# Optimization experiments

Measured on AMD Instinct MI355X. Metric: run time of the kernel, lower is better.

## Reference

```python
import jax, jax.numpy as jnp
import numpy as np

NUM_HEADS = 16


def setup_inputs() -> dict:
    key = jax.random.key(0)
    ks = jax.random.split(key, 5)
    B, S, D = 4, 2048, 1024
    scale = 1.0 / np.sqrt(D)
    return {
        "x": jax.random.normal(ks[0], (B, S, D), dtype=jnp.float32),
        "q_proj": jax.random.normal(ks[1], (D, D), dtype=jnp.float32) * scale,
        "k_proj": jax.random.normal(ks[2], (D, D), dtype=jnp.float32) * scale,
        "v_proj": jax.random.normal(ks[3], (D, D), dtype=jnp.float32) * scale,
        "o_proj": jax.random.normal(ks[4], (D, D), dtype=jnp.float32) * scale,
    }


def reference(x, q_proj, k_proj, v_proj, o_proj):
    B, S, D = x.shape
    H = NUM_HEADS
    hd = D // H
    # projections: weight is [d_out, d_in]
    q = jnp.einsum('bsd,kd->bsk', x, q_proj)
    k = jnp.einsum('bsd,kd->bsk', x, k_proj)
    v = jnp.einsum('bsd,kd->bsk', x, v_proj)
    # split heads: [B, H, S, hd]
    q = q.reshape(B, S, H, hd).transpose(0, 2, 1, 3)
    k = k.reshape(B, S, H, hd).transpose(0, 2, 1, 3)
    v = v.reshape(B, S, H, hd).transpose(0, 2, 1, 3)
    scores = jnp.einsum('bhqd,bhkd->bhqk', q, k) / jnp.sqrt(jnp.asarray(hd, dtype=x.dtype))
    causal = jnp.tril(jnp.ones((S, S), dtype=bool))  # True = keep
    scores = jnp.where(causal, scores, -jnp.inf)
    attn = jax.nn.softmax(scores, axis=-1)
    out = jnp.einsum('bhqk,bhkd->bhqd', attn, v)
    out = out.transpose(0, 2, 1, 3).reshape(B, S, D)
    return jnp.einsum('bsv,mv->bsm', out, o_proj)
```

## Files before the change

### kernel.cpp

```cpp
#include <hip/hip_runtime.h>
#include <hip/hip_bf16.h>
#include <stdint.h>


typedef __bf16 bf16x8 __attribute__((ext_vector_type(8)));
typedef __bf16 bf16x4 __attribute__((ext_vector_type(4)));
typedef float  f32x4  __attribute__((ext_vector_type(4)));

static __device__ __forceinline__ f32x4 mfma16(bf16x8 a, bf16x8 b, f32x4 c) {
  return __builtin_amdgcn_mfma_f32_16x16x32_bf16(a, b, c, 0, 0, 0);
}

static __device__ __forceinline__ void load16_lds(const void* g, void* l) {
  __builtin_amdgcn_global_load_lds(
      (const __attribute__((address_space(1))) unsigned int*)g,
      (__attribute__((address_space(3))) unsigned int*)l, 16, 0, 0);
}

__global__ __launch_bounds__(256) void cvt_all(
    const float* __restrict__ x,
    const float* __restrict__ w0, const float* __restrict__ w1,
    const float* __restrict__ w2, const float* __restrict__ w3,
    __bf16* __restrict__ xb, __bf16* __restrict__ wqk,
    __bf16* __restrict__ wvb, __bf16* __restrict__ wob) {
  const int blk = blockIdx.x;
  const int t = threadIdx.x;
  if (blk < 4096) {
    int i = blk * 256 + t;
    const float4* in4 = (const float4*)x;
    float4 a = in4[2 * i], b = in4[2 * i + 1];
    __bf16 v[8];
    v[0] = (__bf16)a.x; v[1] = (__bf16)a.y; v[2] = (__bf16)a.z; v[3] = (__bf16)a.w;
    v[4] = (__bf16)b.x; v[5] = (__bf16)b.y; v[6] = (__bf16)b.z; v[7] = (__bf16)b.w;
    *(bf16x8*)(xb + 8 * i) = *(bf16x8*)v;
  } else {
    int b2 = blk - 4096;
    int m = b2 >> 9;
    const float* src = (m == 0) ? w0 : (m == 1) ? w1 : (m == 2) ? w2 : w3;
    __bf16* dst = (m == 0) ? wqk : (m == 1) ? (wqk + (size_t)(1024 * 1024))
                : (m == 2) ? wvb : wob;
    const float scl = (m == 0) ? 0.18033688011112042f : 1.0f;
    int i = (b2 & 511) * 256 + t;
    const float4* in4 = (const float4*)src;
    float4 a = in4[2 * i], b = in4[2 * i + 1];
    __bf16 v[8];
    v[0] = (__bf16)(a.x * scl); v[1] = (__bf16)(a.y * scl);
    v[2] = (__bf16)(a.z * scl); v[3] = (__bf16)(a.w * scl);
    v[4] = (__bf16)(b.x * scl); v[5] = (__bf16)(b.y * scl);
    v[6] = (__bf16)(b.z * scl); v[7] = (__bf16)(b.w * scl);
    *(bf16x8*)(dst + 8 * i) = *(bf16x8*)v;
  }
}

static __device__ __forceinline__ void stage_unit(
    const __bf16* __restrict__ X, long grow0, int K, long k0,
    __bf16* lds, int t) {
  const int lane = t & 63, w = t >> 6;
  const int rl = w * 8 + (lane >> 3);
  const int chunk = (lane & 7) ^ ((lane >> 3) & 7);
  load16_lds(X + (grow0 + rl) * (long)K + k0 + chunk * 8,
             lds + (w * 8) * 64);
}

template <typename OutT>
static __device__ __forceinline__ void gemm_core(
    const __bf16* __restrict__ A, const __bf16* __restrict__ Bw,
    OutT* __restrict__ C, int N, int K, long m0, long n0, int t) {
  __shared__ __align__(16) __bf16 As[3][256 * 64];
  __shared__ __align__(16) __bf16 Bs[3][128 * 64];
  const int lane = t & 63, w = t >> 6;
  const int wm = w >> 1, wn = w & 1;
  const int l15 = lane & 15, quad = lane >> 4;

  int aoff[4][2], boff[4][2];
#pragma unroll
  for (int mf = 0; mf < 4; mf++)
#pragma unroll
    for (int ks = 0; ks < 2; ks++)
      aoff[mf][ks] = (wm * 64 + mf * 16 + l15) * 64 + (((ks * 4 + quad) ^ (l15 & 7)) << 3);
#pragma unroll
  for (int nf = 0; nf < 4; nf++)
#pragma unroll
    for (int ks = 0; ks < 2; ks++)
      boff[nf][ks] = (wn * 64 + nf * 16 + l15) * 64 + (((ks * 4 + quad) ^ (l15 & 7)) << 3);

  const int NT = K >> 6;
  __bf16 *Ac = As[0], *An = As[1], *Asg = As[2];
  __bf16 *Bc = Bs[0], *Bn = Bs[1], *Bsg = Bs[2];

#pragma unroll
  for (int u = 0; u < 4; u++) stage_unit(A, m0 + u * 64, K, 0, Ac + u * 64 * 64, t);
#pragma unroll
  for (int u = 0; u < 2; u++) stage_unit(Bw, n0 + u * 64, K, 0, Bc + u * 64 * 64, t);
#pragma unroll
  for (int u = 0; u < 4; u++) stage_unit(A, m0 + u * 64, K, 64, An + u * 64 * 64, t);
#pragma unroll
  for (int u = 0; u < 2; u++) stage_unit(Bw, n0 + u * 64, K, 64, Bn + u * 64 * 64, t);
  asm volatile("s_waitcnt vmcnt(6)" ::: "memory");
  __builtin_amdgcn_s_barrier();

  f32x4 acc[4][4] = {};
  for (int T = 0; T < NT; T++) {
    const bool pf2 = (T + 2 < NT);
    const long kn2 = (long)(T + 2) * 64;

    bf16x8 bfr[4][2];
#pragma unroll
    for (int nf = 0; nf < 4; nf++)
#pragma unroll
      for (int ks = 0; ks < 2; ks++)
        bfr[nf][ks] = *(const bf16x8*)(Bc + boff[nf][ks]);
    {
      bf16x8 a00 = *(const bf16x8*)(Ac + aoff[0][0]);
      bf16x8 a01 = *(const bf16x8*)(Ac + aoff[0][1]);
      bf16x8 a10 = *(const bf16x8*)(Ac + aoff[1][0]);
      bf16x8 a11 = *(const bf16x8*)(Ac + aoff[1][1]);
      if (pf2) {
#pragma unroll
        for (int u = 0; u < 4; u++)
          stage_unit(A, m0 + u * 64, K, kn2, Asg + u * 64 * 64, t);
      }
      __builtin_amdgcn_s_barrier();
      asm volatile("s_waitcnt lgkmcnt(0)" ::: "memory");
      __builtin_amdgcn_sched_barrier(0);
      __builtin_amdgcn_s_setprio(1);
#pragma unroll
      for (int nf = 0; nf < 4; nf++) {
        acc[0][nf] = mfma16(a00, bfr[nf][0], acc[0][nf]);
        acc[0][nf] = mfma16(a01, bfr[nf][1], acc[0][nf]);
        acc[1][nf] = mfma16(a10, bfr[nf][0], acc[1][nf]);
        acc[1][nf] = mfma16(a11, bfr[nf][1], acc[1][nf]);
      }
      __builtin_amdgcn_s_setprio(0);
      __builtin_amdgcn_s_barrier();
    }
    {
      bf16x8 a00 = *(const bf16x8*)(Ac + aoff[2][0]);
      bf16x8 a01 = *(const bf16x8*)(Ac + aoff[2][1]);
      bf16x8 a10 = *(const bf16x8*)(Ac + aoff[3][0]);
      bf16x8 a11 = *(const bf16x8*)(Ac + aoff[3][1]);
      if (pf2) {
#pragma unroll
        for (int u = 0; u < 2; u++)
          stage_unit(Bw, n0 + u * 64, K, kn2, Bsg + u * 64 * 64, t);
        asm volatile("s_waitcnt vmcnt(6)" ::: "memory");
      } else {
        asm volatile("s_waitcnt vmcnt(0)" ::: "memory");
      }
      __builtin_amdgcn_s_barrier();
      asm volatile("s_waitcnt lgkmcnt(0)" ::: "memory");
      __builtin_amdgcn_sched_barrier(0);
      __builtin_amdgcn_s_setprio(1);
#pragma unroll
      for (int nf = 0; nf < 4; nf++) {
        acc[2][nf] = mfma16(a00, bfr[nf][0], acc[2][nf]);
        acc[2][nf] = mfma16(a01, bfr[nf][1], acc[2][nf]);
        acc[3][nf] = mfma16(a10, bfr[nf][0], acc[3][nf]);
        acc[3][nf] = mfma16(a11, bfr[nf][1], acc[3][nf]);
      }
      __builtin_amdgcn_s_setprio(0);
      __builtin_amdgcn_s_barrier();
    }
    __bf16* ta = Ac; Ac = An; An = Asg; Asg = ta;
    __bf16* tb = Bc; Bc = Bn; Bn = Bsg; Bsg = tb;
  }

#pragma unroll
  for (int mf = 0; mf < 4; mf++)
#pragma unroll
    for (int nf = 0; nf < 4; nf++)
#pragma unroll
      for (int r = 0; r < 4; r++) {
        long row = m0 + wm * 64 + mf * 16 + quad * 4 + r;
        long col = n0 + wn * 64 + nf * 16 + l15;
        float v = acc[mf][nf][r];
        if constexpr (sizeof(OutT) == 2) C[row * (long)N + col] = (OutT)(__bf16)v;
        else                             C[row * (long)N + col] = v;
      }
}

__global__ __launch_bounds__(512, 2) void gemm_dual(
    const __bf16* __restrict__ xb, const __bf16* __restrict__ wqk,
    const __bf16* __restrict__ wvb,
    __bf16* __restrict__ QK, __bf16* __restrict__ VTg) {
  const int bid = blockIdx.x;
  const int swz = (bid & 7) * 96 + (bid >> 3);
  if (swz < 512) {
    gemm_core<__bf16>(xb, wqk, QK, 2048, 1024,
                      (long)(swz / 16) * 256, (long)(swz % 16) * 128, threadIdx.x);
  } else {
    const int s = swz - 512;
    gemm_core<__bf16>(wvb, xb, VTg, 8192, 1024,
                      (long)(s / 64) * 256, (long)(s % 64) * 128, threadIdx.x);
  }
}

__global__ __launch_bounds__(512, 2) void gemm_bt8(
    const __bf16* __restrict__ A, const __bf16* __restrict__ Bw,
    float* __restrict__ C, int M, int N, int K, int NX) {
  const int bid = blockIdx.x;
  const int cpx = gridDim.x >> 3;
  const int swz = (bid & 7) * cpx + (bid >> 3);
  gemm_core<float>(A, Bw, C, N, K, (long)(swz / NX) * 256, (long)(swz % NX) * 128,
                   threadIdx.x);
}

__global__ __launch_bounds__(512, 2) void attn6(
    const __bf16* __restrict__ QK, const __bf16* __restrict__ VT,
    __bf16* __restrict__ O) {
  constexpr int SD = 2048;
  constexpr int LDP = 72;
  __shared__ __align__(16) __bf16 Ks[3][64 * 64];
  __shared__ __align__(16) __bf16 Vs[3][64 * 64];
  __shared__ __align__(16) __bf16 Pw[8 * 32 * LDP];
  const int t = threadIdx.x;
  const int lane = t & 63, w = t >> 6;
  const int l15 = lane & 15, quad = lane >> 4;

  const int bid = blockIdx.x;
  const int g = (bid & 7) * 8 + (bid >> 5);
  const int jj = (bid >> 3) & 3;
  const int h = g & 15, b = g >> 4;

  const long qbase = (long)b * 2048 * SD + h * 64;
  const long kbase = qbase + 1024;
  __bf16* Pme = Pw + w * 32 * LDP;

  const int sr = t >> 3;
  const int scg = (t & 7) ^ (sr & 7);
  const int ldsOff = (w * 8) * 64;
  const __bf16* gK = QK + kbase + (long)sr * SD + scg * 8;
  const __bf16* gV = VT + (long)(h * 64 + sr) * 8192 + b * 2048 + scg * 8;

  int kvoff[4][2];
#pragma unroll
  for (int nt = 0; nt < 4; nt++)
#pragma unroll
    for (int kk = 0; kk < 2; kk++)
      kvoff[nt][kk] = (nt * 16 + l15) * 64 + (((kk * 4 + quad) ^ (l15 & 7)) << 3);

  bf16x8 ones;
#pragma unroll
  for (int j = 0; j < 8; j++) ones[j] = (__bf16)1.0f;

#pragma unroll
  for (int half = 0; half < 2; half++) {
    const int qb = half ? (7 - jj) : jj;
    const int q0 = qb * 256;
    const int wrow0 = q0 + w * 32;

    bf16x8 qf[2][2];
#pragma unroll
    for (int mt = 0; mt < 2; mt++)
#pragma unroll
      for (int kk = 0; kk < 2; kk++)
        qf[mt][kk] = *(const bf16x8*)(QK + qbase +
            (long)(wrow0 + mt * 16 + l15) * SD + kk * 32 + quad * 8);

    f32x4 o_acc[2][4] = {};
    f32x4 o_l[2] = {};

    const int nkt = 4 * qb + 4;

    __syncthreads();
    load16_lds(gK, Ks[0] + ldsOff);
    load16_lds(gV, Vs[0] + ldsOff);
    load16_lds(gK + (long)64 * SD, Ks[1] + ldsOff);
    load16_lds(gV + 64, Vs[1] + ldsOff);

    int cur = 0;
    for (int kt = 0; kt < nkt; kt++) {
      if (kt + 1 < nkt) asm volatile("s_waitcnt vmcnt(2)" ::: "memory");
      else              asm volatile("s_waitcnt vmcnt(0)" ::: "memory");
      __builtin_amdgcn_s_barrier();
      __builtin_amdgcn_sched_barrier(0);

      if (kt + 2 < nkt) {
        int stg = cur + 2; if (stg >= 3) stg -= 3;
        load16_lds(gK + (long)(kt + 2) * 64 * SD, Ks[stg] + ldsOff);
        load16_lds(gV + (kt + 2) * 64, Vs[stg] + ldsOff);
      }

      const int k0 = kt * 64;
      if (k0 <= wrow0 + 31) {
        const __bf16* KsB = Ks[cur];
        const __bf16* VsB = Vs[cur];
        bf16x8 kf[4][2];
#pragma unroll
        for (int nt = 0; nt < 4; nt++)
#pragma unroll
          for (int kk = 0; kk < 2; kk++)
            kf[nt][kk] = *(const bf16x8*)(KsB + kvoff[nt][kk]);
        f32x4 st[4][2];
        __builtin_amdgcn_s_setprio(1);
#pragma unroll
        for (int nt = 0; nt < 4; nt++)
#pragma unroll
          for (int mt = 0; mt < 2; mt++) {
            f32x4 z = {0.f, 0.f, 0.f, 0.f};
            z = mfma16(kf[nt][0], qf[mt][0], z);
            st[nt][mt] = mfma16(kf[nt][1], qf[mt][1], z);
          }
        __builtin_amdgcn_s_setprio(0);

        if (k0 + 63 <= wrow0) {
#pragma unroll
          for (int mt = 0; mt < 2; mt++)
#pragma unroll
            for (int nt = 0; nt < 4; nt++) {
              bf16x4 pb;
#pragma unroll
              for (int r = 0; r < 4; r++)
                pb[r] = (__bf16)__builtin_amdgcn_exp2f(st[nt][mt][r]);
              *(bf16x4*)(Pme + (mt * 16 + l15) * LDP + nt * 16 + quad * 4) = pb;
            }
        } else {
#pragma unroll
          for (int mt = 0; mt < 2; mt++) {
            const int qrow = wrow0 + mt * 16 + l15;
#pragma unroll
            for (int nt = 0; nt < 4; nt++) {
              const int keyb = k0 + nt * 16 + quad * 4;
              bf16x4 pb;
#pragma unroll
              for (int r = 0; r < 4; r++) {
                float e = __builtin_amdgcn_exp2f(st[nt][mt][r]);
                if (keyb + r > qrow) e = 0.f;
                pb[r] = (__bf16)e;
              }
              *(bf16x4*)(Pme + (mt * 16 + l15) * LDP + nt * 16 + quad * 4) = pb;
            }
          }
        }

#pragma unroll
        for (int kk = 0; kk < 2; kk++) {
          bf16x8 vf[4];
#pragma unroll
          for (int dt = 0; dt < 4; dt++)
            vf[dt] = *(const bf16x8*)(VsB + kvoff[dt][kk]);
#pragma unroll
          for (int mt = 0; mt < 2; mt++) {
            bf16x8 pf = *(const bf16x8*)(Pme + (mt * 16 + l15) * LDP + kk * 32 + quad * 8);
            __builtin_amdgcn_s_setprio(1);
#pragma unroll
            for (int dt = 0; dt < 4; dt++)
              o_acc[mt][dt] = mfma16(pf, vf[dt], o_acc[mt][dt]);
            o_l[mt] = mfma16(pf, ones, o_l[mt]);
            __builtin_amdgcn_s_setprio(0);
          }
        }
      }
      cur = (cur == 2) ? 0 : cur + 1;
    }

#pragma unroll
    for (int mt = 0; mt < 2; mt++) {
#pragma unroll
      for (int r = 0; r < 4; r++) {
        float inv = 1.f / o_l[mt][r];
        int row = wrow0 + mt * 16 + quad * 4 + r;
        long ob = ((long)b * 2048 + row) * 1024 + h * 64;
#pragma unroll
        for (int dt = 0; dt < 4; dt++)
          O[ob + dt * 16 + l15] = (__bf16)(o_acc[mt][dt][r] * inv);
      }
    }
  }
}

extern "C" void kernel_launch(void* const* d_in, const int* in_sizes, int n_in,
                              void* d_out, int out_size, void* d_ws, size_t ws_size,
                              hipStream_t stream) {
  const float* x  = (const float*)d_in[0];
  const float* wq = (const float*)d_in[1];
  const float* wk = (const float*)d_in[2];
  const float* wv = (const float*)d_in[3];
  const float* wo = (const float*)d_in[4];
  float* out = (float*)d_out;

  char* ws = (char*)d_ws;
  __bf16* xb   = (__bf16*)(ws);
  __bf16* wqk  = (__bf16*)(ws + (16l << 20));
  __bf16* wvb  = (__bf16*)(ws + (20l << 20));
  __bf16* wob  = (__bf16*)(ws + (22l << 20));
  __bf16* QK   = (__bf16*)(ws + (24l << 20));
  __bf16* VTg  = (__bf16*)(ws + (56l << 20));
  __bf16* Ab   = xb;

  cvt_all<<<6144, 256, 0, stream>>>(x, wq, wk, wv, wo, xb, wqk, wvb, wob);

  gemm_dual<<<768, 512, 0, stream>>>(xb, wqk, wvb, QK, VTg);

  attn6<<<256, 512, 0, stream>>>(QK, VTg, Ab);

  gemm_bt8<<<256, 512, 0, stream>>>(Ab, wob, out, 8192, 1024, 1024, 8);
}
```

Baseline: 227.5 us.

## Split attention into one q-tile per block, heaviest first, with double buffering

Attention now runs one 256-row query tile per block over 512 blocks. Before, 256 blocks each processed a paired short and long q-tile. Blocks are ordered so the largest causal tiles launch first, which aims for better load balance and more parallel work across CUs. The KV pipeline drops from triple to double buffering with a full vmcnt(0) wait each iteration. That lowers LDS use but exposes more load latency per step.

New measurement: 227.7 us. About the same (+0.1%).

```diff
diff --git a/kernel.cpp b/kernel.cpp
--- a/kernel.cpp
+++ b/kernel.cpp
@@ -205,21 +205,21 @@
                    threadIdx.x);
 }
 
-__global__ __launch_bounds__(512, 2) void attn6(
+__global__ __launch_bounds__(512, 2) void attn8(
     const __bf16* __restrict__ QK, const __bf16* __restrict__ VT,
     __bf16* __restrict__ O) {
   constexpr int SD = 2048;
   constexpr int LDP = 72;
-  __shared__ __align__(16) __bf16 Ks[3][64 * 64];
-  __shared__ __align__(16) __bf16 Vs[3][64 * 64];
+  __shared__ __align__(16) __bf16 Ks[2][64 * 64];
+  __shared__ __align__(16) __bf16 Vs[2][64 * 64];
   __shared__ __align__(16) __bf16 Pw[8 * 32 * LDP];
   const int t = threadIdx.x;
   const int lane = t & 63, w = t >> 6;
   const int l15 = lane & 15, quad = lane >> 4;
 
   const int bid = blockIdx.x;
-  const int g = (bid & 7) * 8 + (bid >> 5);
-  const int jj = (bid >> 3) & 3;
+  const int qt = 7 - (bid >> 6);
+  const int g = (bid & 7) * 8 + ((bid >> 3) & 7);
   const int h = g & 15, b = g >> 4;
 
   const long qbase = (long)b * 2048 * SD + h * 64;
@@ -243,128 +243,118 @@
 #pragma unroll
   for (int j = 0; j < 8; j++) ones[j] = (__bf16)1.0f;
 
-#pragma unroll
-  for (int half = 0; half < 2; half++) {
-    const int qb = half ? (7 - jj) : jj;
-    const int q0 = qb * 256;
-    const int wrow0 = q0 + w * 32;
-
-    bf16x8 qf[2][2];
-#pragma unroll
-    for (int mt = 0; mt < 2; mt++)
-#pragma unroll
-      for (int kk = 0; kk < 2; kk++)
-        qf[mt][kk] = *(const bf16x8*)(QK + qbase +
-            (long)(wrow0 + mt * 16 + l15) * SD + kk * 32 + quad * 8);
-
-    f32x4 o_acc[2][4] = {};
-    f32x4 o_l[2] = {};
-
-    const int nkt = 4 * qb + 4;
-
-    __syncthreads();
-    load16_lds(gK, Ks[0] + ldsOff);
-    load16_lds(gV, Vs[0] + ldsOff);
-    load16_lds(gK + (long)64 * SD, Ks[1] + ldsOff);
-    load16_lds(gV + 64, Vs[1] + ldsOff);
-
-    int cur = 0;
-    for (int kt = 0; kt < nkt; kt++) {
-      if (kt + 1 < nkt) asm volatile("s_waitcnt vmcnt(2)" ::: "memory");
-      else              asm volatile("s_waitcnt vmcnt(0)" ::: "memory");
-      __builtin_amdgcn_s_barrier();
-      __builtin_amdgcn_sched_barrier(0);
-
-      if (kt + 2 < nkt) {
-        int stg = cur + 2; if (stg >= 3) stg -= 3;
-        load16_lds(gK + (long)(kt + 2) * 64 * SD, Ks[stg] + ldsOff);
-        load16_lds(gV + (kt + 2) * 64, Vs[stg] + ldsOff);
-      }
-
-      const int k0 = kt * 64;
-      if (k0 <= wrow0 + 31) {
-        const __bf16* KsB = Ks[cur];
-        const __bf16* VsB = Vs[cur];
-        bf16x8 kf[4][2];
-#pragma unroll
-        for (int nt = 0; nt < 4; nt++)
-#pragma unroll
-          for (int kk = 0; kk < 2; kk++)
-            kf[nt][kk] = *(const bf16x8*)(KsB + kvoff[nt][kk]);
-        f32x4 st[4][2];
-        __builtin_amdgcn_s_setprio(1);
-#pragma unroll
-        for (int nt = 0; nt < 4; nt++)
-#pragma unroll
-          for (int mt = 0; mt < 2; mt++) {
-            f32x4 z = {0.f, 0.f, 0.f, 0.f};
-            z = mfma16(kf[nt][0], qf[mt][0], z);
-            st[nt][mt] = mfma16(kf[nt][1], qf[mt][1], z);
+  const int q0 = qt * 256;
+  const int wrow0 = q0 + w * 32;
+
+  bf16x8 qf[2][2];
+#pragma unroll
+  for (int mt = 0; mt < 2; mt++)
+#pragma unroll
+    for (int kk = 0; kk < 2; kk++)
+      qf[mt][kk] = *(const bf16x8*)(QK + qbase +
+          (long)(wrow0 + mt * 16 + l15) * SD + kk * 32 + quad * 8);
+
+  f32x4 o_acc[2][4] = {};
+  f32x4 o_l[2] = {};
+
+  const int nkt = 4 * qt + 4;
+
+  load16_lds(gK, Ks[0] + ldsOff);
+  load16_lds(gV, Vs[0] + ldsOff);
+
+  for (int kt = 0; kt < nkt; kt++) {
+    const int cur = kt & 1;
+    asm volatile("s_waitcnt vmcnt(0)" ::: "memory");
+    __builtin_amdgcn_s_barrier();
+    __builtin_amdgcn_sched_barrier(0);
+
+    if (kt + 1 < nkt) {
+      load16_lds(gK + (long)(kt + 1) * 64 * SD, Ks[cur ^ 1] + ldsOff);
+      load16_lds(gV + (kt + 1) * 64, Vs[cur ^ 1] + ldsOff);
+    }
+
+    const int k0 = kt * 64;
+    if (k0 <= wrow0 + 31) {
+      const __bf16* KsB = Ks[cur];
+      const __bf16* VsB = Vs[cur];
+      bf16x8 kf[4][2];
+#pragma unroll
+      for (int nt = 0; nt < 4; nt++)
+#pragma unroll
+        for (int kk = 0; kk < 2; kk++)
+          kf[nt][kk] = *(const bf16x8*)(KsB + kvoff[nt][kk]);
+      f32x4 st[4][2];
+      __builtin_amdgcn_s_setprio(1);
+#pragma unroll
+      for (int nt = 0; nt < 4; nt++)
+#pragma unroll
+        for (int mt = 0; mt < 2; mt++) {
+          f32x4 z = {0.f, 0.f, 0.f, 0.f};
+          z = mfma16(kf[nt][0], qf[mt][0], z);
+          st[nt][mt] = mfma16(kf[nt][1], qf[mt][1], z);
+        }
+      __builtin_amdgcn_s_setprio(0);
+
+      if (k0 + 63 <= wrow0) {
+#pragma unroll
+        for (int mt = 0; mt < 2; mt++)
+#pragma unroll
+          for (int nt = 0; nt < 4; nt++) {
+            bf16x4 pb;
+#pragma unroll
+            for (int r = 0; r < 4; r++)
+              pb[r] = (__bf16)__builtin_amdgcn_exp2f(st[nt][mt][r]);
+            *(bf16x4*)(Pme + (mt * 16 + l15) * LDP + nt * 16 + quad * 4) = pb;
           }
-        __builtin_amdgcn_s_setprio(0);
-
-        if (k0 + 63 <= wrow0) {
-#pragma unroll
-          for (int mt = 0; mt < 2; mt++)
-#pragma unroll
-            for (int nt = 0; nt < 4; nt++) {
-              bf16x4 pb;
-#pragma unroll
-              for (int r = 0; r < 4; r++)
-                pb[r] = (__bf16)__builtin_amdgcn_exp2f(st[nt][mt][r]);
-              *(bf16x4*)(Pme + (mt * 16 + l15) * LDP + nt * 16 + quad * 4) = pb;
+      } else {
+#pragma unroll
+        for (int mt = 0; mt < 2; mt++) {
+          const int qrow = wrow0 + mt * 16 + l15;
+#pragma unroll
+          for (int nt = 0; nt < 4; nt++) {
+            const int keyb = k0 + nt * 16 + quad * 4;
+            bf16x4 pb;
+#pragma unroll
+            for (int r = 0; r < 4; r++) {
+              float e = __builtin_amdgcn_exp2f(st[nt][mt][r]);
+              if (keyb + r > qrow) e = 0.f;
+              pb[r] = (__bf16)e;
             }
-        } else {
-#pragma unroll
-          for (int mt = 0; mt < 2; mt++) {
-            const int qrow = wrow0 + mt * 16 + l15;
-#pragma unroll
-            for (int nt = 0; nt < 4; nt++) {
-              const int keyb = k0 + nt * 16 + quad * 4;
-              bf16x4 pb;
-#pragma unroll
-              for (int r = 0; r < 4; r++) {
-                float e = __builtin_amdgcn_exp2f(st[nt][mt][r]);
-                if (keyb + r > qrow) e = 0.f;
-                pb[r] = (__bf16)e;
-              }
-              *(bf16x4*)(Pme + (mt * 16 + l15) * LDP + nt * 16 + quad * 4) = pb;
-            }
+            *(bf16x4*)(Pme + (mt * 16 + l15) * LDP + nt * 16 + quad * 4) = pb;
           }
         }
-
-#pragma unroll
-        for (int kk = 0; kk < 2; kk++) {
-          bf16x8 vf[4];
+      }
+
+#pragma unroll
+      for (int kk = 0; kk < 2; kk++) {
+        bf16x8 vf[4];
+#pragma unroll
+        for (int dt = 0; dt < 4; dt++)
+          vf[dt] = *(const bf16x8*)(VsB + kvoff[dt][kk]);
+#pragma unroll
+        for (int mt = 0; mt < 2; mt++) {
+          bf16x8 pf = *(const bf16x8*)(Pme + (mt * 16 + l15) * LDP + kk * 32 + quad * 8);
+          __builtin_amdgcn_s_setprio(1);
 #pragma unroll
           for (int dt = 0; dt < 4; dt++)
-            vf[dt] = *(const bf16x8*)(VsB + kvoff[dt][kk]);
-#pragma unroll
-          for (int mt = 0; mt < 2; mt++) {
-            bf16x8 pf = *(const bf16x8*)(Pme + (mt * 16 + l15) * LDP + kk * 32 + quad * 8);
-            __builtin_amdgcn_s_setprio(1);
-#pragma unroll
-            for (int dt = 0; dt < 4; dt++)
-              o_acc[mt][dt] = mfma16(pf, vf[dt], o_acc[mt][dt]);
-            o_l[mt] = mfma16(pf, ones, o_l[mt]);
-            __builtin_amdgcn_s_setprio(0);
-          }
+            o_acc[mt][dt] = mfma16(pf, vf[dt], o_acc[mt][dt]);
+          o_l[mt] = mfma16(pf, ones, o_l[mt]);
+          __builtin_amdgcn_s_setprio(0);
         }
       }
-      cur = (cur == 2) ? 0 : cur + 1;
-    }
-
-#pragma unroll
-    for (int mt = 0; mt < 2; mt++) {
-#pragma unroll
-      for (int r = 0; r < 4; r++) {
-        float inv = 1.f / o_l[mt][r];
-        int row = wrow0 + mt * 16 + quad * 4 + r;
-        long ob = ((long)b * 2048 + row) * 1024 + h * 64;
-#pragma unroll
-        for (int dt = 0; dt < 4; dt++)
-          O[ob + dt * 16 + l15] = (__bf16)(o_acc[mt][dt][r] * inv);
-      }
+    }
+  }
+
+#pragma unroll
+  for (int mt = 0; mt < 2; mt++) {
+#pragma unroll
+    for (int r = 0; r < 4; r++) {
+      float inv = 1.f / o_l[mt][r];
+      int row = wrow0 + mt * 16 + quad * 4 + r;
+      long ob = ((long)b * 2048 + row) * 1024 + h * 64;
+#pragma unroll
+      for (int dt = 0; dt < 4; dt++)
+        O[ob + dt * 16 + l15] = (__bf16)(o_acc[mt][dt][r] * inv);
     }
   }
 }
@@ -392,7 +382,7 @@
 
   gemm_dual<<<768, 512, 0, stream>>>(xb, wqk, wvb, QK, VTg);
 
-  attn6<<<256, 512, 0, stream>>>(QK, VTg, Ab);
+  attn8<<<512, 512, 0, stream>>>(QK, VTg, Ab);
 
   gemm_bt8<<<256, 512, 0, stream>>>(Ab, wob, out, 8192, 1024, 1024, 8);
 }
```

## Use 256x256 tiles for QK projection GEMM with shared LDS buffer

Applied to the files above, without the earlier changes.

Adds a 256x256-tile GEMM core (8 waves as 2x4, each owning 128x64) for the fused Q/K projection. It double-buffers A and B in LDS and interleaves the global loads with the MFMA sub-steps. The V-projection path keeps the 256x128 core, and both paths now draw on one externally provided shared buffer, so the merged launch shrinks from 768 to 512 blocks. Larger tiles raise arithmetic intensity and cut redundant loads of A, at the cost of more accumulator registers and a shallower prefetch pipeline for A.

After: 240.4 us. 1.06x slower.

```diff
diff --git a/kernel.cpp b/kernel.cpp
--- a/kernel.cpp
+++ b/kernel.cpp
@@ -65,9 +65,10 @@
 template <typename OutT>
 static __device__ __forceinline__ void gemm_core(
     const __bf16* __restrict__ A, const __bf16* __restrict__ Bw,
-    OutT* __restrict__ C, int N, int K, long m0, long n0, int t) {
-  __shared__ __align__(16) __bf16 As[3][256 * 64];
-  __shared__ __align__(16) __bf16 Bs[3][128 * 64];
+    OutT* __restrict__ C, int N, int K, long m0, long n0,
+    __bf16* smem, int t) {
+  __bf16* Asb = smem;
+  __bf16* Bsb = smem + 49152;
   const int lane = t & 63, w = t >> 6;
   const int wm = w >> 1, wn = w & 1;
   const int l15 = lane & 15, quad = lane >> 4;
@@ -85,8 +86,8 @@
       boff[nf][ks] = (wn * 64 + nf * 16 + l15) * 64 + (((ks * 4 + quad) ^ (l15 & 7)) << 3);
 
   const int NT = K >> 6;
-  __bf16 *Ac = As[0], *An = As[1], *Asg = As[2];
-  __bf16 *Bc = Bs[0], *Bn = Bs[1], *Bsg = Bs[2];
+  __bf16 *Ac = Asb, *An = Asb + 16384, *Asg = Asb + 32768;
+  __bf16 *Bc = Bsb, *Bn = Bsb + 8192,  *Bsg = Bsb + 16384;
 
 #pragma unroll
   for (int u = 0; u < 4; u++) stage_unit(A, m0 + u * 64, K, 0, Ac + u * 64 * 64, t);
@@ -179,30 +180,192 @@
       }
 }
 
-__global__ __launch_bounds__(512, 2) void gemm_dual(
+template <typename OutT>
+static __device__ __forceinline__ void gemm_core256(
+    const __bf16* __restrict__ A, const __bf16* __restrict__ Bw,
+    OutT* __restrict__ C, int N, int K, long m0, long n0,
+    __bf16* smem, int t) {
+  __bf16* Asp[2] = {smem, smem + 16384};
+  __bf16* Bsp[2] = {smem + 32768, smem + 49152};
+  const int lane = t & 63, w = t >> 6;
+  const int wm = w >> 2, wn = w & 3;
+  const int l15 = lane & 15, quad = lane >> 4;
+
+  int aoff[8][2], boff[4][2];
+#pragma unroll
+  for (int mf = 0; mf < 8; mf++)
+#pragma unroll
+    for (int ks = 0; ks < 2; ks++)
+      aoff[mf][ks] = (wm * 128 + mf * 16 + l15) * 64 + (((ks * 4 + quad) ^ (l15 & 7)) << 3);
+#pragma unroll
+  for (int nf = 0; nf < 4; nf++)
+#pragma unroll
+    for (int ks = 0; ks < 2; ks++)
+      boff[nf][ks] = (wn * 64 + nf * 16 + l15) * 64 + (((ks * 4 + quad) ^ (l15 & 7)) << 3);
+
+  const int NT = K >> 6;
+#pragma unroll
+  for (int u = 0; u < 4; u++) stage_unit(A,  m0 + u * 64, K, 0,  Asp[0] + u * 4096, t);
+#pragma unroll
+  for (int u = 0; u < 4; u++) stage_unit(Bw, n0 + u * 64, K, 0,  Bsp[0] + u * 4096, t);
+#pragma unroll
+  for (int u = 0; u < 4; u++) stage_unit(Bw, n0 + u * 64, K, 64, Bsp[1] + u * 4096, t);
+  asm volatile("s_waitcnt vmcnt(4)" ::: "memory");
+  __builtin_amdgcn_s_barrier();
+
+  f32x4 acc[8][4] = {};
+  for (int T = 0; T < NT; T++) {
+    const int cur = T & 1;
+    __bf16* Ac = Asp[cur];
+    __bf16* Bc = Bsp[cur];
+    __bf16* An = Asp[cur ^ 1];
+    const bool pf1 = (T + 1 < NT);
+    const bool pf2 = (T + 2 < NT);
+    const long kn1 = (long)(T + 1) * 64;
+    const long kn2 = (long)(T + 2) * 64;
+
+    bf16x8 bfr[4][2];
+
+    if (pf1) {
+#pragma unroll
+      for (int u = 0; u < 4; u++) stage_unit(A, m0 + u * 64, K, kn1, An + u * 4096, t);
+    }
+#pragma unroll
+    for (int nf = 0; nf < 4; nf++)
+#pragma unroll
+      for (int ks = 0; ks < 2; ks++)
+        bfr[nf][ks] = *(const bf16x8*)(Bc + boff[nf][ks]);
+    {
+      bf16x8 a00 = *(const bf16x8*)(Ac + aoff[0][0]);
+      bf16x8 a01 = *(const bf16x8*)(Ac + aoff[0][1]);
+      bf16x8 a10 = *(const bf16x8*)(Ac + aoff[1][0]);
+      bf16x8 a11 = *(const bf16x8*)(Ac + aoff[1][1]);
+      __builtin_amdgcn_s_barrier();
+      asm volatile("s_waitcnt lgkmcnt(0)" ::: "memory");
+      __builtin_amdgcn_sched_barrier(0);
+      __builtin_amdgcn_s_setprio(1);
+#pragma unroll
+      for (int nf = 0; nf < 4; nf++) {
+        acc[0][nf] = mfma16(a00, bfr[nf][0], acc[0][nf]);
+        acc[0][nf] = mfma16(a01, bfr[nf][1], acc[0][nf]);
+        acc[1][nf] = mfma16(a10, bfr[nf][0], acc[1][nf]);
+        acc[1][nf] = mfma16(a11, bfr[nf][1], acc[1][nf]);
+      }
+      __builtin_amdgcn_s_setprio(0);
+      __builtin_amdgcn_s_barrier();
+    }
+    if (pf2) {
+#pragma unroll
+      for (int u = 0; u < 2; u++) stage_unit(Bw, n0 + u * 64, K, kn2, Bc + u * 4096, t);
+    }
+    {
+      bf16x8 a00 = *(const bf16x8*)(Ac + aoff[2][0]);
+      bf16x8 a01 = *(const bf16x8*)(Ac + aoff[2][1]);
+      bf16x8 a10 = *(const bf16x8*)(Ac + aoff[3][0]);
+      bf16x8 a11 = *(const bf16x8*)(Ac + aoff[3][1]);
+      __builtin_amdgcn_s_barrier();
+      asm volatile("s_waitcnt lgkmcnt(0)" ::: "memory");
+      __builtin_amdgcn_sched_barrier(0);
+      __builtin_amdgcn_s_setprio(1);
+#pragma unroll
+      for (int nf = 0; nf < 4; nf++) {
+        acc[2][nf] = mfma16(a00, bfr[nf][0], acc[2][nf]);
+        acc[2][nf] = mfma16(a01, bfr[nf][1], acc[2][nf]);
+        acc[3][nf] = mfma16(a10, bfr[nf][0], acc[3][nf]);
+        acc[3][nf] = mfma16(a11, bfr[nf][1], acc[3][nf]);
+      }
+      __builtin_amdgcn_s_setprio(0);
+      __builtin_amdgcn_s_barrier();
+    }
+    if (pf2) {
+#pragma unroll
+      for (int u = 2; u < 4; u++) stage_unit(Bw, n0 + u * 64, K, kn2, Bc + u * 4096, t);
+    }
+    {
+      bf16x8 a00 = *(const bf16x8*)(Ac + aoff[4][0]);
+      bf16x8 a01 = *(const bf16x8*)(Ac + aoff[4][1]);
+      bf16x8 a10 = *(const bf16x8*)(Ac + aoff[5][0]);
+      bf16x8 a11 = *(const bf16x8*)(Ac + aoff[5][1]);
+      __builtin_amdgcn_s_barrier();
+      asm volatile("s_waitcnt lgkmcnt(0)" ::: "memory");
+      __builtin_amdgcn_sched_barrier(0);
+      __builtin_amdgcn_s_setprio(1);
+#pragma unroll
+      for (int nf = 0; nf < 4; nf++) {
+        acc[4][nf] = mfma16(a00, bfr[nf][0], acc[4][nf]);
+        acc[4][nf] = mfma16(a01, bfr[nf][1], acc[4][nf]);
+        acc[5][nf] = mfma16(a10, bfr[nf][0], acc[5][nf]);
+        acc[5][nf] = mfma16(a11, bfr[nf][1], acc[5][nf]);
+      }
+      __builtin_amdgcn_s_setprio(0);
+      __builtin_amdgcn_s_barrier();
+    }
+    {
+      bf16x8 a00 = *(const bf16x8*)(Ac + aoff[6][0]);
+      bf16x8 a01 = *(const bf16x8*)(Ac + aoff[6][1]);
+      bf16x8 a10 = *(const bf16x8*)(Ac + aoff[7][0]);
+      bf16x8 a11 = *(const bf16x8*)(Ac + aoff[7][1]);
+      if (pf2)      asm volatile("s_waitcnt vmcnt(4)" ::: "memory");
+      else if (pf1) asm volatile("s_waitcnt vmcnt(0)" ::: "memory");
+      __builtin_amdgcn_s_barrier();
+      asm volatile("s_waitcnt lgkmcnt(0)" ::: "memory");
+      __builtin_amdgcn_sched_barrier(0);
+      __builtin_amdgcn_s_setprio(1);
+#pragma unroll
+      for (int nf = 0; nf < 4; nf++) {
+        acc[6][nf] = mfma16(a00, bfr[nf][0], acc[6][nf]);
+        acc[6][nf] = mfma16(a01, bfr[nf][1], acc[6][nf]);
+        acc[7][nf] = mfma16(a10, bfr[nf][0], acc[7][nf]);
+        acc[7][nf] = mfma16(a11, bfr[nf][1], acc[7][nf]);
+      }
+      __builtin_amdgcn_s_setprio(0);
+      __builtin_amdgcn_s_barrier();
+    }
+  }
+
+#pragma unroll
+  for (int mf = 0; mf < 8; mf++)
+#pragma unroll
+    for (int nf = 0; nf < 4; nf++)
+#pragma unroll
+      for (int r = 0; r < 4; r++) {
+        long row = m0 + wm * 128 + mf * 16 + quad * 4 + r;
+        long col = n0 + wn * 64 + nf * 16 + l15;
+        float v = acc[mf][nf][r];
+        if constexpr (sizeof(OutT) == 2) C[row * (long)N + col] = (OutT)(__bf16)v;
+        else                             C[row * (long)N + col] = v;
+      }
+}
+
+__global__ __launch_bounds__(512, 2) void gemm_in(
     const __bf16* __restrict__ xb, const __bf16* __restrict__ wqk,
     const __bf16* __restrict__ wvb,
     __bf16* __restrict__ QK, __bf16* __restrict__ VTg) {
+  __shared__ __align__(16) __bf16 smem[73728];
   const int bid = blockIdx.x;
-  const int swz = (bid & 7) * 96 + (bid >> 3);
-  if (swz < 512) {
-    gemm_core<__bf16>(xb, wqk, QK, 2048, 1024,
-                      (long)(swz / 16) * 256, (long)(swz % 16) * 128, threadIdx.x);
+  if (bid < 256) {
+    const int swz = (bid & 7) * 32 + (bid >> 3);
+    gemm_core256<__bf16>(xb, wqk, QK, 2048, 1024,
+                         (long)(swz >> 3) * 256, (long)(swz & 7) * 256,
+                         smem, threadIdx.x);
   } else {
-    const int s = swz - 512;
+    const int b2 = bid - 256;
+    const int swz = (b2 & 7) * 32 + (b2 >> 3);
     gemm_core<__bf16>(wvb, xb, VTg, 8192, 1024,
-                      (long)(s / 64) * 256, (long)(s % 64) * 128, threadIdx.x);
+                      (long)(swz >> 6) * 256, (long)(swz & 63) * 128,
+                      smem, threadIdx.x);
   }
 }
 
 __global__ __launch_bounds__(512, 2) void gemm_bt8(
     const __bf16* __restrict__ A, const __bf16* __restrict__ Bw,
     float* __restrict__ C, int M, int N, int K, int NX) {
+  __shared__ __align__(16) __bf16 smem[73728];
   const int bid = blockIdx.x;
   const int cpx = gridDim.x >> 3;
   const int swz = (bid & 7) * cpx + (bid >> 3);
   gemm_core<float>(A, Bw, C, N, K, (long)(swz / NX) * 256, (long)(swz % NX) * 128,
-                   threadIdx.x);
+                   smem, threadIdx.x);
 }
 
 __global__ __launch_bounds__(512, 2) void attn6(
@@ -390,7 +553,7 @@
 
   cvt_all<<<6144, 256, 0, stream>>>(x, wq, wk, wv, wo, xb, wqk, wvb, wob);
 
-  gemm_dual<<<768, 512, 0, stream>>>(xb, wqk, wvb, QK, VTg);
+  gemm_in<<<512, 512, 0, stream>>>(xb, wqk, wvb, QK, VTg);
 
   attn6<<<256, 512, 0, stream>>>(QK, VTg, Ab);
 
```
